# Optimization experiments

Hardware: AMD Instinct MI355X
Metric: run time of the kernel (lower is better)

The kernel has to match this reference:

```python
import jax, jax.numpy as jnp
import numpy as np

SLOPE = 0.01  # LeakyReLU default negative slope
EPS = 1e-5    # BatchNorm eps


def _lrelu(x):
    return jnp.where(x >= 0, x, SLOPE * x)


def _conv(x, w, b):
    # x: [B,C,H,W], w: [O,I,kh,kw] (torch layout)
    y = jax.lax.conv_general_dilated(x, w, (1, 1), 'VALID',
                                     dimension_numbers=('NCHW', 'OIHW', 'NCHW'))
    return y + b[None, :, None, None]


def _bn4(x, p):
    # eval-mode BatchNorm2d; p = [gamma, beta, running_mean, running_var] stacked [4,C]
    g, b, m, v = p
    s = g * jax.lax.rsqrt(v + EPS)
    return x * s[None, :, None, None] + (b - m * s)[None, :, None, None]


def _forward(observation, action, sc1_w, sc1_b, sbn1, sc2_w, sc2_b, sbn2,
             mc1_w, mc1_b, mbn1, mc2_w, mc2_b, mbn2,
             gw_root, gw_rel, g_b, gbn,
             a_cw, a_cb, a_w1, a_b1, a_w2, a_b2, a_w3, a_b3,
             edge_index, edge_type, nodes_to_select):
    # ---- multi-scale temporal CNN (eval mode: dropout = identity) ----
    s = _lrelu(_bn4(_conv(observation, sc1_w, sc1_b), sbn1))
    s = _lrelu(_bn4(_conv(s, sc2_w, sc2_b), sbn2))          # [B,20,N,1]
    m = _lrelu(_bn4(_conv(observation, mc1_w, mc1_b), mbn1))
    m = _lrelu(_bn4(_conv(m, mc2_w, mc2_b), mbn2))          # [B,20,N,1]
    l = _lrelu(jnp.max(observation, axis=3, keepdims=True)) # [B,3,N,1]
    temporal = jnp.concatenate([s, m, l], axis=1)           # [B,43,N,1]

    # ---- RGCN (graph replicated per batch element; aggr='mean' per relation) ----
    x = jnp.swapaxes(temporal[..., 0], 1, 2)                # [B,N,F]
    N = x.shape[1]
    src, dst = edge_index[0], edge_index[1]
    out = jnp.einsum('bnf,fg->bng', x, gw_root) + g_b       # root transform + bias
    for r in range(gw_rel.shape[0]):
        h = jnp.einsum('bnf,fg->bng', x, gw_rel[r])         # per-relation transform
        mask = (edge_type == r).astype(x.dtype)             # [E]
        msgs = h[:, src, :] * mask[None, :, None]           # [B,E,F] gather
        agg = jax.ops.segment_sum(jnp.swapaxes(msgs, 0, 1), dst, num_segments=N)  # [N,B,F]
        deg = jax.ops.segment_sum(mask, dst, num_segments=N)                       # [N]
        out = out + jnp.swapaxes(agg, 0, 1) / jnp.maximum(deg, 1.0)[None, :, None]
    # BatchNorm1d (eval) + LeakyReLU; dropout = identity
    g, be, mu, v = gbn
    sg = g * jax.lax.rsqrt(v + EPS)
    out = _lrelu(out * sg + (be - mu * sg))                 # [B,N,F]

    graph_feats = jnp.swapaxes(out, 1, 2)[..., None]        # [B,F,N,1]
    feats = jnp.concatenate([temporal, graph_feats], axis=1)  # [B,86,N,1]
    feats = feats[:, :, nodes_to_select, :]                 # [B,86,P,1]

    # ---- actor head (mode == 'actor'); cash_bias is zeroed in the original ----
    stocks = action[:, 1:][:, None, :, None]                # [B,1,P,1]
    f = jnp.concatenate([stocks, feats], axis=1)[..., 0]    # [B,87,P]
    logits = jnp.einsum('bcp,c->bp', f, a_cw) + a_cb[0]     # 1x1 conv, out_ch=1
    o = jnp.concatenate([jnp.zeros((f.shape[0], 1), f.dtype), logits], axis=1)  # [B,P+1]
    h1 = jax.nn.relu(o @ a_w1 + a_b1)
    h2 = jax.nn.relu(h1 @ a_w2 + a_b2)
    return jax.nn.softmax(h2 @ a_w3 + a_b3, axis=-1)


def setup_inputs() -> dict:
    key = jax.random.key(0)
    ks = jax.random.split(key, 30)
    B, C0, N, T = 64, 3, 500, 50
    E, R, P, H = 16000, 4, 500, 128
    CM, CF = 3, 20
    F = 2 * CF + C0  # 43

    def rn(k, sh, s=0.1):
        return jax.random.normal(k, sh, jnp.float32) * s

    def bn_p(k, c):
        k1, k2, k3, k4 = jax.random.split(k, 4)
        return jnp.stack([jax.random.uniform(k1, (c,), jnp.float32, 0.5, 1.5),
                          rn(k2, (c,)), rn(k3, (c,)),
                          jax.random.uniform(k4, (c,), jnp.float32, 0.5, 1.5)])

    return {
        'observation': jax.random.normal(ks[0], (B, C0, N, T), jnp.float32),
        'action': jax.random.uniform(ks[1], (B, P + 1), jnp.float32),
        'edge_index': jax.random.randint(ks[2], (2, E), 0, N),
        'edge_type': jax.random.randint(ks[3], (E,), 0, R),
        'nodes_to_select': jnp.arange(P),
        'sc1_w': rn(ks[4], (CM, C0, 1, 3)), 'sc1_b': rn(ks[5], (CM,)), 'sbn1': bn_p(ks[6], CM),
        'sc2_w': rn(ks[7], (CF, CM, 1, 48)), 'sc2_b': rn(ks[8], (CF,)), 'sbn2': bn_p(ks[9], CF),
        'mc1_w': rn(ks[10], (CM, C0, 1, 21)), 'mc1_b': rn(ks[11], (CM,)), 'mbn1': bn_p(ks[12], CM),
        'mc2_w': rn(ks[13], (CF, CM, 1, 30)), 'mc2_b': rn(ks[14], (CF,)), 'mbn2': bn_p(ks[15], CF),
        'gw_root': rn(ks[16], (F, F)), 'gw_rel': rn(ks[17], (R, F, F)),
        'g_b': rn(ks[18], (F,)), 'gbn': bn_p(ks[19], F),
        'a_cw': rn(ks[20], (2 * F + 1,)), 'a_cb': rn(ks[21], (1,)),
        'a_w1': rn(ks[22], (P + 1, H)), 'a_b1': rn(ks[23], (H,)),
        'a_w2': rn(ks[24], (H, H)), 'a_b2': rn(ks[25], (H,)),
        'a_w3': rn(ks[26], (H, P + 1)), 'a_b3': rn(ks[27], (P + 1,)),
    }


def reference(observation, action, edge_index, edge_type, nodes_to_select,
              sc1_w, sc1_b, sbn1, sc2_w, sc2_b, sbn2,
              mc1_w, mc1_b, mbn1, mc2_w, mc2_b, mbn2,
              gw_root, gw_rel, g_b, gbn,
              a_cw, a_cb, a_w1, a_b1, a_w2, a_b2, a_w3, a_b3):
    return _forward(observation, action, sc1_w, sc1_b, sbn1, sc2_w, sc2_b, sbn2,
                    mc1_w, mc1_b, mbn1, mc2_w, mc2_b, mbn2,
                    gw_root, gw_rel, g_b, gbn,
                    a_cw, a_cb, a_w1, a_b1, a_w2, a_b2, a_w3, a_b3,
                    edge_index, edge_type, nodes_to_select)
```

## Files before the change

kernel.cpp:

```cpp
#include <hip/hip_runtime.h>

#define SLOPE 0.01f
#define EPSV  1e-5f
#define BB    64
#define NN    500
#define TT    50
#define E_N   16000
#define FF    43
#define PP    500
#define HH    128
#define XSTRIDE 48

typedef const float* fp;

__device__ __forceinline__ float lrelu(float x){ return x >= 0.f ? x : SLOPE * x; }
__device__ __forceinline__ float bnap(float x, fp bnp, int c, int C){
  float g  = bnp[c], b_ = bnp[C + c];
  float m  = bnp[2*C + c], v = bnp[3*C + c];
  float s = g * rsqrtf(v + EPSV);
  return x * s + (b_ - m * s);
}

__global__ __launch_bounds__(1024) void k_prep15(
    fp sc2w, fp mc2w, fp gwroot, fp gwrel,
    float* __restrict__ wT_s2, float* __restrict__ wT_m2, float* __restrict__ wTg,
    float* __restrict__ o_ws)
{
  int tid = threadIdx.x, blk = blockIdx.x;
  if (blk == 0){
    for (int i = tid; i < 2880; i += 1024){ int o = i/144, x = i%144; wT_s2[x*20+o] = sc2w[i]; }
  } else if (blk == 1){
    for (int i = tid; i < 1800; i += 1024){ int o = i/90,  x = i%90;  wT_m2[x*20+o] = mc2w[i]; }
  } else if (blk < 6){
    for (int i = (blk-2)*1024 + tid; i < 9245; i += 4096){
      int f5 = i/43, g = i%43;
      wTg[i] = (f5 < 43) ? gwroot[f5*43+g] : gwrel[(f5-43)*43+g];
    }
  } else if (blk == 6){
    if (tid < BB) o_ws[tid*(PP+1)] = 0.f;
  } else {
    for (int i = 9245 + tid; i < 9312; i += 1024) wTg[i] = 0.f;
  }
}

__global__ __launch_bounds__(512, 2) void k_tempo15(
    fp obs,
    fp sc1w, fp sc1b, fp sbn1, fp sc2b, fp sbn2,
    fp mc1w, fp mc1b, fp mbn1, fp mc2b, fp mbn2,
    const float* __restrict__ wT_s2, const float* __restrict__ wT_m2,
    float* __restrict__ xbuf,
    const int* __restrict__ ei, const int* __restrict__ et,
    int* __restrict__ begr, int* __restrict__ e_s, float* __restrict__ inv_deg)
{
  __shared__ float smem[11776];
  #define OL(n,j)   smem[(n)*151 + (j)]
  #define PB(w,n,o) smem[(w)*1472 + (n)*23 + (o)]
  int tid = threadIdx.x;

  if (blockIdx.x == 512){
    int* S   = (int*)smem;
    int* cnt = S;
    int* idg = S + 512;
    int* cur = S + 2560;
    for (int i = tid; i < 512;  i += 512) cnt[i] = 0;
    for (int i = tid; i < 2048; i += 512) idg[i] = 0;
    __syncthreads();
    for (int e = tid; e < E_N; e += 512){
      int d = ei[E_N + e], r = et[e];
      atomicAdd(&cnt[d], 1);
      atomicAdd(&idg[r*NN + d], 1);
    }
    __syncthreads();
    for (int off = 1; off < 512; off <<= 1){
      int v = (tid >= off) ? cnt[tid - off] : 0;
      __syncthreads();
      cnt[tid] += v;
      __syncthreads();
    }
    if (tid < NN){
      int o  = tid ? cnt[tid-1] : 0;
      int c1 = o  + idg[tid];
      int c2 = c1 + idg[NN + tid];
      int c3 = c2 + idg[2*NN + tid];
      begr[tid*4+0] = o;  begr[tid*4+1] = c1;
      begr[tid*4+2] = c2; begr[tid*4+3] = c3;
      cur[tid*4+0] = o;  cur[tid*4+1] = c1;
      cur[tid*4+2] = c2; cur[tid*4+3] = c3;
      #pragma unroll
      for (int r = 0; r < 4; r++)
        inv_deg[r*NN+tid] = 1.f / fmaxf((float)idg[r*NN+tid], 1.f);
    }
    if (tid == 0) begr[2000] = E_N;
    __syncthreads();
    for (int e = tid; e < E_N; e += 512){
      int s = ei[e], d = ei[E_N + e], r = et[e];
      int pos = atomicAdd(&cur[d*4 + r], 1);
      e_s[pos] = s;
    }
    return;
  }

  int w = __builtin_amdgcn_readfirstlane(tid >> 6);
  int lane = tid & 63;
  int b  = blockIdx.x >> 3;
  int n0 = (blockIdx.x & 7) << 6;
  int span = (NN - n0 < 64) ? (NN - n0) : 64;

  for (int c = 0; c < 3; c++){
    const float* base = obs + (size_t)(b*3 + c)*25000;
    for (int idx = tid; idx < 3200; idx += 512){
      int n = idx / 50, t = idx % 50;
      int node = n0 + n; if (node > NN-1) node = NN-1;
      OL(n, c*50 + t) = base[node*50 + t];
    }
  }
  __syncthreads();

  float acc[20];
  float mx[3] = {-1e30f, -1e30f, -1e30f};
  if (w < 5){
    int t0 = w * 6;
    float ov[3][26];
    #pragma unroll
    for (int ci = 0; ci < 3; ci++)
      #pragma unroll
      for (int j = 0; j < 26; j++)
        ov[ci][j] = OL(lane, ci*50 + t0 + j);
    float sc1[3], sh1[3];
    #pragma unroll
    for (int ci = 0; ci < 3; ci++){
      float s = mbn1[ci] * rsqrtf(mbn1[9+ci] + EPSV);
      sc1[ci] = s; sh1[ci] = mbn1[3+ci] - mbn1[6+ci]*s;
    }
    #pragma unroll
    for (int o = 0; o < 20; o++) acc[o] = 0.f;
    #pragma unroll
    for (int i = 0; i < 6; i++){
      int tt = t0 + i;
      float mv[3];
      #pragma unroll
      for (int co = 0; co < 3; co++) mv[co] = mc1b[co];
      #pragma unroll
      for (int ci = 0; ci < 3; ci++)
        #pragma unroll
        for (int k = 0; k < 21; k++){
          float v = ov[ci][i + k];
          #pragma unroll
          for (int co = 0; co < 3; co++) mv[co] += v * mc1w[co*63 + ci*21 + k];
        }
      #pragma unroll
      for (int co = 0; co < 3; co++){
        float z = lrelu(mv[co]*sc1[co] + sh1[co]);
        const float* wp = wT_m2 + (co*30 + tt)*20;
        #pragma unroll
        for (int o = 0; o < 20; o++) acc[o] += z * wp[o];
      }
    }
  } else {
    int ws_ = w - 5;
    int t0 = ws_ * 16;
    float ovs[3][18];
    #pragma unroll
    for (int ci = 0; ci < 3; ci++)
      #pragma unroll
      for (int j = 0; j < 18; j++)
        ovs[ci][j] = OL(lane, ci*50 + t0 + j);
    int l0 = ws_ * 17;
    int ln = (50 - l0 < 17) ? (50 - l0) : 17;
    for (int j = 0; j < ln; j++){
      #pragma unroll
      for (int c = 0; c < 3; c++)
        mx[c] = fmaxf(mx[c], OL(lane, c*50 + l0 + j));
    }
    float sc1[3], sh1[3];
    #pragma unroll
    for (int ci = 0; ci < 3; ci++){
      float s = sbn1[ci] * rsqrtf(sbn1[9+ci] + EPSV);
      sc1[ci] = s; sh1[ci] = sbn1[3+ci] - sbn1[6+ci]*s;
    }
    #pragma unroll
    for (int o = 0; o < 20; o++) acc[o] = 0.f;
    #pragma unroll
    for (int i = 0; i < 16; i++){
      int tt = t0 + i;
      float sv[3];
      #pragma unroll
      for (int co = 0; co < 3; co++) sv[co] = sc1b[co];
      #pragma unroll
      for (int ci = 0; ci < 3; ci++)
        #pragma unroll
        for (int k = 0; k < 3; k++){
          float v = ovs[ci][i + k];
          #pragma unroll
          for (int co = 0; co < 3; co++) sv[co] += v * sc1w[co*9 + ci*3 + k];
        }
      #pragma unroll
      for (int co = 0; co < 3; co++){
        float z = lrelu(sv[co]*sc1[co] + sh1[co]);
        const float* wp = wT_s2 + (co*48 + tt)*20;
        #pragma unroll
        for (int o = 0; o < 20; o++) acc[o] += z * wp[o];
      }
    }
  }
  __syncthreads();

  #pragma unroll
  for (int o = 0; o < 20; o++) PB(w, lane, o) = acc[o];
  if (w >= 5){
    #pragma unroll
    for (int c = 0; c < 3; c++) PB(w, lane, 20 + c) = mx[c];
  }
  __syncthreads();

  size_t gx = (size_t)(b*NN + n0)*XSTRIDE;
  for (int idx = tid; idx < 64*20; idx += 512){
    int n = idx / 20, o = idx % 20;
    if (n < span){
      float v = PB(0,n,o) + PB(1,n,o) + PB(2,n,o) + PB(3,n,o) + PB(4,n,o);
      xbuf[gx + (size_t)n*XSTRIDE + 20 + o] = lrelu(bnap(v + mc2b[o], mbn2, o, 20));
    }
  }
  for (int idx = tid; idx < 64*20; idx += 512){
    int n = idx / 20, o = idx % 20;
    if (n < span){
      float v = PB(5,n,o) + PB(6,n,o) + PB(7,n,o);
      xbuf[gx + (size_t)n*XSTRIDE + o] = lrelu(bnap(v + sc2b[o], sbn2, o, 20));
    }
  }
  for (int idx = tid; idx < 64*3; idx += 512){
    int n = idx / 3, c = idx % 3;
    if (n < span){
      float v = fmaxf(fmaxf(PB(5,n,20+c), PB(6,n,20+c)), PB(7,n,20+c));
      xbuf[gx + (size_t)n*XSTRIDE + 40 + c] = lrelu(v);
    }
  }
  #undef OL
  #undef PB
}

__global__ __launch_bounds__(1024) void k_graph15(
    const float* __restrict__ xbuf, const float* __restrict__ wTg,
    fp gb, fp gbnp, const float* __restrict__ inv_deg,
    const int* __restrict__ begr, const int* __restrict__ e_s,
    fp action, fp acw, fp acb,
    float* __restrict__ gbuf, float* __restrict__ o_ws)
{
  __shared__ float xin[64][219];
  __shared__ float lred[16][64];
  int p = blockIdx.x;
  int l = ((p & 7) * 63) + (p >> 3);
  if (l >= 500) return;
  int tid = threadIdx.x;
  int w = tid >> 6, lane = tid & 63;
  int g0 = l * 64;

  for (int q = 0; q < 4; q++){
    int nl = (w << 2) + q;
    int g = __builtin_amdgcn_readfirstlane(g0 + nl);
    int b = g / NN;
    int n = g - b * NN;
    const float* xb = xbuf + (size_t)(b * NN) * XSTRIDE;
    float xv = (lane < FF) ? xbuf[(size_t)g*XSTRIDE + lane] : 0.f;
    float ar[4];
    #pragma unroll
    for (int r = 0; r < 4; r++){
      int beg = __builtin_amdgcn_readfirstlane(begr[n*4 + r]);
      int end = __builtin_amdgcn_readfirstlane(begr[n*4 + r + 1]);
      float a0 = 0.f, a1 = 0.f, a2 = 0.f, a3 = 0.f;
      int i = beg;
      for (; i + 4 <= end; i += 4){
        int s0 = e_s[i], s1 = e_s[i+1], s2 = e_s[i+2], s3 = e_s[i+3];
        float v0 = (lane < FF) ? xb[(size_t)s0*XSTRIDE + lane] : 0.f;
        float v1 = (lane < FF) ? xb[(size_t)s1*XSTRIDE + lane] : 0.f;
        float v2 = (lane < FF) ? xb[(size_t)s2*XSTRIDE + lane] : 0.f;
        float v3 = (lane < FF) ? xb[(size_t)s3*XSTRIDE + lane] : 0.f;
        a0 += v0; a1 += v1; a2 += v2; a3 += v3;
      }
      for (; i < end; i++){
        int s = e_s[i];
        a0 += (lane < FF) ? xb[(size_t)s*XSTRIDE + lane] : 0.f;
      }
      ar[r] = ((a0 + a1) + (a2 + a3)) * inv_deg[r*NN + n];
    }
    if (lane < FF){
      xin[nl][lane]       = xv;
      xin[nl][ 43 + lane] = ar[0];
      xin[nl][ 86 + lane] = ar[1];
      xin[nl][129 + lane] = ar[2];
      xin[nl][172 + lane] = ar[3];
    }
  }
  __syncthreads();

  int c0 = __builtin_amdgcn_readfirstlane(w * 3);
  int g = g0 + lane;
  float acc[3];
  #pragma unroll
  for (int j = 0; j < 3; j++) acc[j] = (c0 + j < FF) ? gb[c0+j] : 0.f;
  for (int f = 0; f < 215; f++){
    float v = xin[lane][f];
    const float* wp = wTg + f*43 + c0;
    #pragma unroll
    for (int j = 0; j < 3; j++) acc[j] += v * wp[j];
  }
  float lp = 0.f;
  #pragma unroll
  for (int j = 0; j < 3; j++){
    int c = c0 + j;
    if (c < FF){
      float gv = lrelu(bnap(acc[j], gbnp, c, FF));
      gbuf[(size_t)g*XSTRIDE + c] = gv;
      lp += gv * acw[1 + FF + c];
    }
  }
  if (w == 15){
    int b = g / NN, n = g - b * NN;
    float xp = acb[0] + action[b*(PP+1) + 1 + n] * acw[0];
    #pragma unroll 2
    for (int c = 0; c < FF; c++) xp += xin[lane][c] * acw[1 + c];
    lp = xp;
  }
  lred[w][lane] = lp;
  __syncthreads();
  if (tid < 64){
    float t = 0.f;
    #pragma unroll
    for (int w2 = 0; w2 < 16; w2++) t += lred[w2][tid];
    int g2 = g0 + tid;
    int b = g2 / NN, n = g2 - b * NN;
    o_ws[b*(PP+1) + 1 + n] = t;
  }
}

__global__ __launch_bounds__(512) void k_fcall(
    const float* __restrict__ o_ws,
    fp aw1, fp ab1, fp aw2, fp ab2, fp aw3, fp ab3,
    float* __restrict__ out)
{
  int b = blockIdx.x;
  int tid = threadIdx.x;
  __shared__ float os[PP+1];
  __shared__ float part[4][HH];
  __shared__ float h1[HH];
  __shared__ float h2[HH];
  __shared__ float red[512];

  if (tid <= PP) os[tid] = o_ws[b*(PP+1) + tid];
  __syncthreads();

  {
    int chunk = tid >> 7, h = tid & 127;
    int k0 = chunk * 125;
    int kn = (chunk == 3) ? 126 : 125;
    float acc = 0.f;
    for (int k = 0; k < kn; k++) acc += os[k0+k] * aw1[(k0+k)*HH + h];
    part[chunk][h] = acc;
  }
  __syncthreads();
  if (tid < HH)
    h1[tid] = fmaxf(ab1[tid] + part[0][tid] + part[1][tid] + part[2][tid] + part[3][tid], 0.f);
  __syncthreads();
  if (tid < HH){
    float acc = ab2[tid];
    #pragma unroll 4
    for (int k = 0; k < HH; k++) acc += h1[k] * aw2[k*HH + tid];
    h2[tid] = fmaxf(acc, 0.f);
  }
  __syncthreads();

  float val = -1e30f;
  if (tid <= PP){
    float acc = ab3[tid];
    #pragma unroll 4
    for (int k = 0; k < HH; k++) acc += h2[k] * aw3[k*(PP+1) + tid];
    val = acc;
  }
  red[tid] = val;
  __syncthreads();
  for (int s = 256; s > 0; s >>= 1){
    if (tid < s) red[tid] = fmaxf(red[tid], red[tid + s]);
    __syncthreads();
  }
  float mxv = red[0];
  __syncthreads();
  float e = (tid <= PP) ? expf(val - mxv) : 0.f;
  red[tid] = e;
  __syncthreads();
  for (int s = 256; s > 0; s >>= 1){
    if (tid < s) red[tid] += red[tid + s];
    __syncthreads();
  }
  float sum = red[0];
  if (tid <= PP) out[b*(PP+1) + tid] = e / sum;
}

extern "C" void kernel_launch(void* const* d_in, const int* in_sizes, int n_in,
                              void* d_out, int out_size, void* d_ws, size_t ws_size,
                              hipStream_t stream)
{
  fp obs    = (fp)d_in[0];
  fp action = (fp)d_in[1];
  const int* ei  = (const int*)d_in[2];
  const int* et  = (const int*)d_in[3];
  fp sc1w=(fp)d_in[5],  sc1b=(fp)d_in[6],  sbn1=(fp)d_in[7];
  fp sc2w=(fp)d_in[8],  sc2b=(fp)d_in[9],  sbn2=(fp)d_in[10];
  fp mc1w=(fp)d_in[11], mc1b=(fp)d_in[12], mbn1=(fp)d_in[13];
  fp mc2w=(fp)d_in[14], mc2b=(fp)d_in[15], mbn2=(fp)d_in[16];
  fp gwroot=(fp)d_in[17], gwrel=(fp)d_in[18], gb=(fp)d_in[19], gbnp=(fp)d_in[20];
  fp acw=(fp)d_in[21], acb=(fp)d_in[22];
  fp aw1=(fp)d_in[23], ab1=(fp)d_in[24];
  fp aw2=(fp)d_in[25], ab2=(fp)d_in[26];
  fp aw3=(fp)d_in[27], ab3=(fp)d_in[28];

  float* xbuf   = (float*)d_ws;
  float* gbuf   = xbuf + 1536000;
  float* wT_s2  = gbuf + 1536000;
  float* wT_m2  = wT_s2 + 2880;
  float* wTg    = wT_m2 + 1800;
  float* invdeg = wTg + 9312;
  float* o_ws   = invdeg + 2000;
  int*   ip     = (int*)(o_ws + 32064);
  int* begr = ip;
  int* e_s  = ip + 2001;

  float* out = (float*)d_out;

  hipLaunchKernelGGL(k_prep15, dim3(8), dim3(1024), 0, stream,
    sc2w, mc2w, gwroot, gwrel, wT_s2, wT_m2, wTg, o_ws);
  hipLaunchKernelGGL(k_tempo15, dim3(513), dim3(512), 0, stream,
    obs, sc1w, sc1b, sbn1, sc2b, sbn2,
    mc1w, mc1b, mbn1, mc2b, mbn2, wT_s2, wT_m2, xbuf,
    ei, et, begr, e_s, invdeg);
  hipLaunchKernelGGL(k_graph15, dim3(504), dim3(1024), 0, stream,
    xbuf, wTg, gb, gbnp, invdeg, begr, e_s, action, acw, acb, gbuf, o_ws);
  hipLaunchKernelGGL(k_fcall, dim3(BB), dim3(512), 0, stream,
    o_ws, aw1, ab1, aw2, ab2, aw3, ab3, out);
}
```

Measured before the change: 257.4 us.

## Replace single-block CSR build with padded per-(node,relation) edge buckets built in prep

Removes the serial single-block CSR construction (histogram, prefix scan, scatter) from the temporal kernel and instead buckets edges in the prep kernel with global atomics into fixed-size padded slots (40 per node-relation), zeroed by a memset. The graph kernel reads counts directly and computes the mean divisor from the count. It also drops the unused gbuf store. This shortens the critical path set by the lone CSR block, but edges beyond 40 per bucket would be silently dropped, and edge order within a bucket is nondeterministic.

```diff
diff --git a/kernel.cpp b/kernel.cpp
--- a/kernel.cpp
+++ b/kernel.cpp
@@ -10,6 +10,7 @@
 #define PP    500
 #define HH    128
 #define XSTRIDE 48
+#define PAD_E 40
 
 typedef const float* fp;
 
@@ -21,10 +22,12 @@
   return x * s + (b_ - m * s);
 }
 
-__global__ __launch_bounds__(1024) void k_prep15(
+__global__ __launch_bounds__(1024) void k_prep16(
     fp sc2w, fp mc2w, fp gwroot, fp gwrel,
     float* __restrict__ wT_s2, float* __restrict__ wT_m2, float* __restrict__ wTg,
-    float* __restrict__ o_ws)
+    float* __restrict__ o_ws,
+    const int* __restrict__ ei, const int* __restrict__ et,
+    int* __restrict__ cntg, int* __restrict__ esp)
 {
   int tid = threadIdx.x, blk = blockIdx.x;
   if (blk == 0){
@@ -38,67 +41,30 @@
     }
   } else if (blk == 6){
     if (tid < BB) o_ws[tid*(PP+1)] = 0.f;
+  } else if (blk == 7){
+    for (int i = 9245 + tid; i < 9312; i += 1024) wTg[i] = 0.f;
   } else {
-    for (int i = 9245 + tid; i < 9312; i += 1024) wTg[i] = 0.f;
-  }
-}
-
-__global__ __launch_bounds__(512, 2) void k_tempo15(
+    int e = (blk - 8)*1024 + tid;
+    if (e < E_N){
+      int s = ei[e], d = ei[E_N + e], r = et[e];
+      int idx = d*4 + r;
+      int pos = atomicAdd(&cntg[idx], 1);
+      if (pos < PAD_E) esp[idx*PAD_E + pos] = s;
+    }
+  }
+}
+
+__global__ __launch_bounds__(512, 2) void k_tempo16(
     fp obs,
     fp sc1w, fp sc1b, fp sbn1, fp sc2b, fp sbn2,
     fp mc1w, fp mc1b, fp mbn1, fp mc2b, fp mbn2,
     const float* __restrict__ wT_s2, const float* __restrict__ wT_m2,
-    float* __restrict__ xbuf,
-    const int* __restrict__ ei, const int* __restrict__ et,
-    int* __restrict__ begr, int* __restrict__ e_s, float* __restrict__ inv_deg)
+    float* __restrict__ xbuf)
 {
   __shared__ float smem[11776];
   #define OL(n,j)   smem[(n)*151 + (j)]
   #define PB(w,n,o) smem[(w)*1472 + (n)*23 + (o)]
   int tid = threadIdx.x;
-
-  if (blockIdx.x == 512){
-    int* S   = (int*)smem;
-    int* cnt = S;
-    int* idg = S + 512;
-    int* cur = S + 2560;
-    for (int i = tid; i < 512;  i += 512) cnt[i] = 0;
-    for (int i = tid; i < 2048; i += 512) idg[i] = 0;
-    __syncthreads();
-    for (int e = tid; e < E_N; e += 512){
-      int d = ei[E_N + e], r = et[e];
-      atomicAdd(&cnt[d], 1);
-      atomicAdd(&idg[r*NN + d], 1);
-    }
-    __syncthreads();
-    for (int off = 1; off < 512; off <<= 1){
-      int v = (tid >= off) ? cnt[tid - off] : 0;
-      __syncthreads();
-      cnt[tid] += v;
-      __syncthreads();
-    }
-    if (tid < NN){
-      int o  = tid ? cnt[tid-1] : 0;
-      int c1 = o  + idg[tid];
-      int c2 = c1 + idg[NN + tid];
-      int c3 = c2 + idg[2*NN + tid];
-      begr[tid*4+0] = o;  begr[tid*4+1] = c1;
-      begr[tid*4+2] = c2; begr[tid*4+3] = c3;
-      cur[tid*4+0] = o;  cur[tid*4+1] = c1;
-      cur[tid*4+2] = c2; cur[tid*4+3] = c3;
-      #pragma unroll
-      for (int r = 0; r < 4; r++)
-        inv_deg[r*NN+tid] = 1.f / fmaxf((float)idg[r*NN+tid], 1.f);
-    }
-    if (tid == 0) begr[2000] = E_N;
-    __syncthreads();
-    for (int e = tid; e < E_N; e += 512){
-      int s = ei[e], d = ei[E_N + e], r = et[e];
-      int pos = atomicAdd(&cur[d*4 + r], 1);
-      e_s[pos] = s;
-    }
-    return;
-  }
 
   int w = __builtin_amdgcn_readfirstlane(tid >> 6);
   int lane = tid & 63;
@@ -239,12 +205,12 @@
   #undef PB
 }
 
-__global__ __launch_bounds__(1024) void k_graph15(
+__global__ __launch_bounds__(1024) void k_graph16(
     const float* __restrict__ xbuf, const float* __restrict__ wTg,
-    fp gb, fp gbnp, const float* __restrict__ inv_deg,
-    const int* __restrict__ begr, const int* __restrict__ e_s,
+    fp gb, fp gbnp,
+    const int* __restrict__ cntg, const int* __restrict__ esp,
     fp action, fp acw, fp acb,
-    float* __restrict__ gbuf, float* __restrict__ o_ws)
+    float* __restrict__ o_ws)
 {
   __shared__ float xin[64][219];
   __shared__ float lred[16][64];
@@ -265,23 +231,25 @@
     float ar[4];
     #pragma unroll
     for (int r = 0; r < 4; r++){
-      int beg = __builtin_amdgcn_readfirstlane(begr[n*4 + r]);
-      int end = __builtin_amdgcn_readfirstlane(begr[n*4 + r + 1]);
+      int idx = n*4 + r;
+      int c = __builtin_amdgcn_readfirstlane(cntg[idx]);
+      if (c > PAD_E) c = PAD_E;
+      const int* ep = esp + idx*PAD_E;
       float a0 = 0.f, a1 = 0.f, a2 = 0.f, a3 = 0.f;
-      int i = beg;
-      for (; i + 4 <= end; i += 4){
-        int s0 = e_s[i], s1 = e_s[i+1], s2 = e_s[i+2], s3 = e_s[i+3];
+      int i = 0;
+      for (; i + 4 <= c; i += 4){
+        int s0 = ep[i], s1 = ep[i+1], s2 = ep[i+2], s3 = ep[i+3];
         float v0 = (lane < FF) ? xb[(size_t)s0*XSTRIDE + lane] : 0.f;
         float v1 = (lane < FF) ? xb[(size_t)s1*XSTRIDE + lane] : 0.f;
         float v2 = (lane < FF) ? xb[(size_t)s2*XSTRIDE + lane] : 0.f;
         float v3 = (lane < FF) ? xb[(size_t)s3*XSTRIDE + lane] : 0.f;
         a0 += v0; a1 += v1; a2 += v2; a3 += v3;
       }
-      for (; i < end; i++){
-        int s = e_s[i];
+      for (; i < c; i++){
+        int s = ep[i];
         a0 += (lane < FF) ? xb[(size_t)s*XSTRIDE + lane] : 0.f;
       }
-      ar[r] = ((a0 + a1) + (a2 + a3)) * inv_deg[r*NN + n];
+      ar[r] = ((a0 + a1) + (a2 + a3)) / fmaxf((float)c, 1.f);
     }
     if (lane < FF){
       xin[nl][lane]       = xv;
@@ -294,7 +262,6 @@
   __syncthreads();
 
   int c0 = __builtin_amdgcn_readfirstlane(w * 3);
-  int g = g0 + lane;
   float acc[3];
   #pragma unroll
   for (int j = 0; j < 3; j++) acc[j] = (c0 + j < FF) ? gb[c0+j] : 0.f;
@@ -310,11 +277,11 @@
     int c = c0 + j;
     if (c < FF){
       float gv = lrelu(bnap(acc[j], gbnp, c, FF));
-      gbuf[(size_t)g*XSTRIDE + c] = gv;
       lp += gv * acw[1 + FF + c];
     }
   }
   if (w == 15){
+    int g = g0 + lane;
     int b = g / NN, n = g - b * NN;
     float xp = acb[0] + action[b*(PP+1) + 1 + n] * acw[0];
     #pragma unroll 2
@@ -414,26 +381,23 @@
   fp aw3=(fp)d_in[27], ab3=(fp)d_in[28];
 
   float* xbuf   = (float*)d_ws;
-  float* gbuf   = xbuf + 1536000;
-  float* wT_s2  = gbuf + 1536000;
+  float* wT_s2  = xbuf + 1536000;
   float* wT_m2  = wT_s2 + 2880;
   float* wTg    = wT_m2 + 1800;
-  float* invdeg = wTg + 9312;
-  float* o_ws   = invdeg + 2000;
-  int*   ip     = (int*)(o_ws + 32064);
-  int* begr = ip;
-  int* e_s  = ip + 2001;
+  float* o_ws   = wTg + 9312;
+  int*   cntg   = (int*)(o_ws + 32064);
+  int*   esp    = cntg + 2000;
 
   float* out = (float*)d_out;
 
-  hipLaunchKernelGGL(k_prep15, dim3(8), dim3(1024), 0, stream,
-    sc2w, mc2w, gwroot, gwrel, wT_s2, wT_m2, wTg, o_ws);
-  hipLaunchKernelGGL(k_tempo15, dim3(513), dim3(512), 0, stream,
+  hipMemsetAsync(cntg, 0, 2000*sizeof(int), stream);
+  hipLaunchKernelGGL(k_prep16, dim3(24), dim3(1024), 0, stream,
+    sc2w, mc2w, gwroot, gwrel, wT_s2, wT_m2, wTg, o_ws, ei, et, cntg, esp);
+  hipLaunchKernelGGL(k_tempo16, dim3(512), dim3(512), 0, stream,
     obs, sc1w, sc1b, sbn1, sc2b, sbn2,
-    mc1w, mc1b, mbn1, mc2b, mbn2, wT_s2, wT_m2, xbuf,
-    ei, et, begr, e_s, invdeg);
-  hipLaunchKernelGGL(k_graph15, dim3(504), dim3(1024), 0, stream,
-    xbuf, wTg, gb, gbnp, invdeg, begr, e_s, action, acw, acb, gbuf, o_ws);
+    mc1w, mc1b, mbn1, mc2b, mbn2, wT_s2, wT_m2, xbuf);
+  hipLaunchKernelGGL(k_graph16, dim3(504), dim3(1024), 0, stream,
+    xbuf, wTg, gb, gbnp, cntg, esp, action, acw, acb, o_ws);
   hipLaunchKernelGGL(k_fcall, dim3(BB), dim3(512), 0, stream,
     o_ws, aw1, ab1, aw2, ab2, aw3, ab3, out);
 }
```

Measured after the change: 248.8 us. 1.03x faster.
